# Kernel tuning notes

Measured on AMD Instinct MI355X. Metric: run time of the kernel, lower is better.

## Reference

```python
import jax, jax.numpy as jnp
import numpy as np

B, T, E, V, L, BLK = 2, 2048, 1024, 32000, 12, 2048


def setup_inputs() -> dict:
    key = jax.random.key(0)
    ks = jax.random.split(key, 10)
    std = 0.005  # FHE-friendly tiny init, matches nn.init.normal_(std=0.005)
    init = lambda k, shape: jax.random.normal(k, shape, jnp.float32) * std
    return {
        "idx": jax.random.randint(ks[0], (B, T), 0, V, dtype=jnp.int32),
        "wte": init(ks[1], (V, E)),
        "wpe": init(ks[2], (BLK, E)),
        "ln1_w": jnp.ones((L, E), jnp.float32),   # FHELayerNorm weights init to ones
        "Wq": init(ks[3], (L, E, E)),
        "Wk": init(ks[4], (L, E, E)),
        "Wv": init(ks[5], (L, E, E)),
        "Wo": init(ks[6], (L, E, E)),
        "ln2_w": jnp.ones((L, E), jnp.float32),
        "fc1": init(ks[7], (L, 2 * E, E)),
        "fc2": init(ks[8], (L, E, 2 * E)),
        "lnf_w": jnp.ones((E,), jnp.float32),
        "lm_head": init(ks[9], (V, E)),
    }


def reference(idx, wte, wpe, ln1_w, Wq, Wk, Wv, Wo, ln2_w, fc1, fc2, lnf_w, lm_head):
    t = idx.shape[1]
    # embeddings, each scaled by 0.01
    x = wte[idx] * 0.01 + (wpe[:t] * 0.01)[None, :, :]  # [B,T,E]

    n_layer = ln1_w.shape[0]
    # inter-block rescale: 0.1 after every block except the last
    scales = jnp.where(jnp.arange(n_layer) < n_layer - 1, 0.1, 1.0).astype(x.dtype)

    def block(x, p):
        ln1, wq, wk, wv, wo, ln2, f1, f2, s = p
        # FHELayerNorm: pure scaling
        h = x * ln1 * 0.1
        # attention (single head over full E, softmax-free quadratic weights)
        q = jnp.einsum('bte,fe->btf', h, wq) * 0.01
        k = jnp.einsum('bte,fe->btf', h, wk) * 0.01
        v = jnp.einsum('bte,fe->btf', h, wv) * 0.1
        a = jnp.einsum('btf,bsf->bts', q, k) * 0.01      # [B,T,T]
        a = a * a * 0.1 + a * 0.1                         # pointwise quadratic
        ao = jnp.einsum('bts,bsf->btf', a, v) * 0.01
        attn_out = jnp.einsum('btf,ef->bte', ao, wo) * 0.1
        x = (x * 0.5 + attn_out * 0.5) * 0.1
        # MLP with polynomial activation
        h2 = x * ln2 * 0.1
        m = jnp.einsum('bte,fe->btf', h2, f1) * 0.05      # [B,T,2E]
        m = m * m * 0.1 + m * 0.1
        m = jnp.einsum('btf,ef->bte', m, f2) * 0.05
        x = (x * 0.5 + m * 0.5) * 0.1
        return x * s, None

    x, _ = jax.lax.scan(block, x, (ln1_w, Wq, Wk, Wv, Wo, ln2_w, fc1, fc2, scales))
    x = x * lnf_w * 0.1  # final FHELayerNorm
    logits = jnp.einsum('bte,ve->btv', x, lm_head) * 0.5
    return logits
```

## Files before the change

kernel.cpp:

```cpp
#include <hip/hip_runtime.h>
#include <hip/hip_fp8.h>
#include <stdint.h>
#include <math.h>

typedef unsigned short u16;
typedef __attribute__((ext_vector_type(4))) float f32x4;
typedef __attribute__((ext_vector_type(2))) long long llx2;

typedef __attribute__((address_space(1))) const uint32_t gas_u32;
typedef __attribute__((address_space(3))) uint32_t las_u32;

__device__ __forceinline__ uint8_t f8(float x) {
  __hip_fp8_e4m3 t(x);
  return (uint8_t)t.__x;
}
__device__ __forceinline__ int ipos(int k) {
  return (k & ~63) | (k & 7) | ((k & 32) >> 2) | ((k & 24) << 1);
}

__device__ __forceinline__ void gl_lds16(const void* g, void* l) {
  __builtin_amdgcn_global_load_lds((gas_u32*)g, (las_u32*)l, 16, 0, 0);
}
__device__ __forceinline__ void barrier_raw() {
  asm volatile("" ::: "memory");
  __builtin_amdgcn_s_barrier();
  asm volatile("" ::: "memory");
}

#define MM8(A_, B_, C_) __builtin_amdgcn_mfma_f32_16x16x32_fp8_fp8(A_, B_, C_, 0, 0, 0)

#define PHASE_MID() do { \
  asm volatile("s_waitcnt lgkmcnt(0)" ::: "memory"); \
  __builtin_amdgcn_sched_barrier(0); \
  __builtin_amdgcn_s_setprio(1); \
} while (0)
#define PHASE_END() do { \
  __builtin_amdgcn_s_setprio(0); \
  __builtin_amdgcn_sched_barrier(0); \
  barrier_raw(); \
} while (0)

__device__ __forceinline__ void xcd_swz(int nwg, int orig, int gx, int& bx, int& by) {
  const int xcd = orig & 7, rem = orig >> 3;
  const int qq = nwg >> 3, rr = nwg & 7;
  const int wg = (xcd < rr ? xcd * (qq + 1) : rr * (qq + 1) + (xcd - rr) * qq) + rem;
  bx = wg % gx; by = wg / gx;
}

struct GP8 {
  const uint8_t* A; long long asb;
  const uint8_t* B[3]; long long bsb;
  uint8_t* O[3]; long long osb;
  int K, lda, ldb, ldo;
  float m1[3], m2[3];
  int epi[3];
  int nsel, msel, nfirst;
  float qc;
  float* xres; const float* lnw; float rscale; float oscale;
  uint8_t* h8out;
  float* fout; int ldf;
};

#define S8A(q, kh, t) do { \
  gl_lds16(gA0 + (size_t)(t) * 128 + (kh) * 64, lAw + (q) * 32768 + (kh) * 8192); \
  gl_lds16(gA1 + (size_t)(t) * 128 + (kh) * 64, lAw + (q) * 32768 + (kh) * 8192 + 4096); \
} while (0)
#define S8B(q, kh, t) do { \
  gl_lds16(gB0 + (size_t)(t) * 128 + (kh) * 64, lBw + (q) * 32768 + (kh) * 8192); \
  gl_lds16(gB1 + (size_t)(t) * 128 + (kh) * 64, lBw + (q) * 32768 + (kh) * 8192 + 4096); \
} while (0)

#define MF8() do { \
  acc[0][0]=MM8(a0[0],b0[0],acc[0][0]); acc[0][0]=MM8(a0[1],b0[1],acc[0][0]); \
  acc[0][1]=MM8(a0[0],b1[0],acc[0][1]); acc[0][1]=MM8(a0[1],b1[1],acc[0][1]); \
  acc[0][2]=MM8(a0[0],b2[0],acc[0][2]); acc[0][2]=MM8(a0[1],b2[1],acc[0][2]); \
  acc[0][3]=MM8(a0[0],b3[0],acc[0][3]); acc[0][3]=MM8(a0[1],b3[1],acc[0][3]); \
  acc[1][0]=MM8(a1[0],b0[0],acc[1][0]); acc[1][0]=MM8(a1[1],b0[1],acc[1][0]); \
  acc[1][1]=MM8(a1[0],b1[0],acc[1][1]); acc[1][1]=MM8(a1[1],b1[1],acc[1][1]); \
  acc[1][2]=MM8(a1[0],b2[0],acc[1][2]); acc[1][2]=MM8(a1[1],b2[1],acc[1][2]); \
  acc[1][3]=MM8(a1[0],b3[0],acc[1][3]); acc[1][3]=MM8(a1[1],b3[1],acc[1][3]); \
  acc[2][0]=MM8(a2[0],b0[0],acc[2][0]); acc[2][0]=MM8(a2[1],b0[1],acc[2][0]); \
  acc[2][1]=MM8(a2[0],b1[0],acc[2][1]); acc[2][1]=MM8(a2[1],b1[1],acc[2][1]); \
  acc[2][2]=MM8(a2[0],b2[0],acc[2][2]); acc[2][2]=MM8(a2[1],b2[1],acc[2][2]); \
  acc[2][3]=MM8(a2[0],b3[0],acc[2][3]); acc[2][3]=MM8(a2[1],b3[1],acc[2][3]); \
  acc[3][0]=MM8(a3[0],b0[0],acc[3][0]); acc[3][0]=MM8(a3[1],b0[1],acc[3][0]); \
  acc[3][1]=MM8(a3[0],b1[0],acc[3][1]); acc[3][1]=MM8(a3[1],b1[1],acc[3][1]); \
  acc[3][2]=MM8(a3[0],b2[0],acc[3][2]); acc[3][2]=MM8(a3[1],b2[1],acc[3][2]); \
  acc[3][3]=MM8(a3[0],b3[0],acc[3][3]); acc[3][3]=MM8(a3[1],b3[1],acc[3][3]); \
} while (0)

__global__ __launch_bounds__(256, 2) void gemm8_k(GP8 p) {
  extern __shared__ __attribute__((aligned(16))) char lds[];
  const int z = blockIdx.z;
  int bx, by;
  xcd_swz(gridDim.x * gridDim.y, blockIdx.y * gridDim.x + blockIdx.x, gridDim.x, bx, by);
  const int m0 = p.nfirst ? by * 128 : bx * 128;
  const int n0 = p.nfirst ? bx * 128 : by * 128;
  const int zi = p.nsel ? (n0 >> 10) : 0;
  const int nB = p.nsel ? (n0 & 1023) : n0;
  const uint8_t* __restrict__ Ap = p.A + (size_t)z * p.asb;
  const uint8_t* __restrict__ Bp = p.B[zi] + (size_t)(p.msel ? (m0 >> 11) : z) * p.bsb;

  const int tid = threadIdx.x, wid = tid >> 6, lane = tid & 63;
  const int wm = wid >> 1, wn = wid & 1;
  const int l15 = lane & 15, l4 = lane >> 4;
  const int cswz16 = (l4 ^ ((l15 >> 1) & 3)) * 16;

  const f32x4 vzero = {0.f, 0.f, 0.f, 0.f};
  f32x4 acc[4][4];
#pragma unroll
  for (int i = 0; i < 4; ++i)
#pragma unroll
    for (int j = 0; j < 4; ++j) acc[i][j] = vzero;

  const int sr = lane >> 2;
  const int cgB = ((lane & 3) ^ ((lane >> 3) & 3)) * 16;
  const uint8_t* gA0 = Ap + (size_t)(m0 + wid * 16 + sr) * p.lda + cgB;
  const uint8_t* gA1 = gA0 + (size_t)64 * p.lda;
  const uint8_t* gB0 = Bp + (size_t)(nB + wid * 16 + sr) * p.ldb + cgB;
  const uint8_t* gB1 = gB0 + (size_t)64 * p.ldb;
  char* lAw = lds + wid * 1024;
  char* lBw = lds + 16384 + wid * 1024;

  const int nt = p.K >> 7;

  S8A(0, 0, 0); S8B(0, 0, 0); S8A(0, 1, 0); S8B(0, 1, 0);
  S8A(1, 0, 1); S8B(1, 0, 1);
  asm volatile("s_waitcnt vmcnt(4)" ::: "memory");
  barrier_raw();

  llx2 a0, a1, a2, a3, b0, b1, b2, b3;
  for (int t = 0; t < nt; ++t) {
    const int q = t & 1;
    const char* Abase = lds + q * 32768 + (wm * 64 + l15) * 64 + cswz16;
    const char* Bbase = lds + q * 32768 + 16384 + (wn * 64 + l15) * 64 + cswz16;
    a0 = *(const llx2*)Abase;          a1 = *(const llx2*)(Abase + 1024);
    a2 = *(const llx2*)(Abase + 2048); a3 = *(const llx2*)(Abase + 3072);
    b0 = *(const llx2*)Bbase;          b1 = *(const llx2*)(Bbase + 1024);
    b2 = *(const llx2*)(Bbase + 2048); b3 = *(const llx2*)(Bbase + 3072);
    if (t + 1 < nt) { S8A(q ^ 1, 1, t + 1); S8B(q ^ 1, 1, t + 1); }
    PHASE_MID(); MF8(); PHASE_END();
    a0 = *(const llx2*)(Abase + 8192);        a1 = *(const llx2*)(Abase + 8192 + 1024);
    a2 = *(const llx2*)(Abase + 8192 + 2048); a3 = *(const llx2*)(Abase + 8192 + 3072);
    b0 = *(const llx2*)(Bbase + 8192);        b1 = *(const llx2*)(Bbase + 8192 + 1024);
    b2 = *(const llx2*)(Bbase + 8192 + 2048); b3 = *(const llx2*)(Bbase + 8192 + 3072);
    if (t + 2 < nt) { S8A(q, 0, t + 2); S8B(q, 0, t + 2); }
    PHASE_MID(); MF8();
    __builtin_amdgcn_s_setprio(0);
    __builtin_amdgcn_sched_barrier(0);
    if (t + 2 < nt) asm volatile("s_waitcnt vmcnt(4)" ::: "memory");
    else            asm volatile("s_waitcnt vmcnt(0)" ::: "memory");
    barrier_raw();
  }

  const int epi = p.epi[zi];
  const float m1v = p.m1[zi], m2v = p.m2[zi];
  uint8_t* __restrict__ Op = p.O[zi] + (size_t)z * p.osb;
#pragma unroll
  for (int mi = 0; mi < 4; ++mi) {
    const int rbase = m0 + wm * 64 + mi * 16 + l4 * 4;
#pragma unroll
    for (int ni = 0; ni < 4; ++ni) {
      const int col = nB + wn * 64 + ni * 16 + l15;
      f32x4 v = acc[mi][ni];
      if (epi == 0) {
#pragma unroll
        for (int r = 0; r < 4; ++r) {
          float y = (v[r] * m1v) * m2v;
          Op[(size_t)(rbase + r) * p.ldo + ipos(col)] = f8(y);
        }
      } else if (epi == 1) {
        const int b = rbase >> 11, rb = rbase & 2047;
        uint32_t pk = 0;
#pragma unroll
        for (int r = 0; r < 4; ++r) {
          float y = (v[r] * m1v) * m2v;
          pk |= (uint32_t)f8(y) << (8 * r);
        }
        *(uint32_t*)(Op + (size_t)b * 2097152 + (size_t)col * 2048 + ipos(rb)) = pk;
      } else if (epi == 2) {
#pragma unroll
        for (int r = 0; r < 4; ++r) {
          float u = (v[r] * m1v) * m2v;
          Op[(size_t)(rbase + r) * p.ldo + ipos(col)] = f8(u * u * p.qc + u);
        }
      } else if (epi == 3) {
#pragma unroll
        for (int r = 0; r < 4; ++r) {
          float add = (v[r] * m1v) * m2v;
          size_t ix = (size_t)(rbase + r) * 1024 + col;
          float xn = (p.xres[ix] + add) * p.rscale;
          p.xres[ix] = xn;
          float hv = xn * p.lnw[col] * 0.1f;
          p.h8out[(size_t)(rbase + r) * 1024 + ipos(col)] = f8(hv * p.oscale);
        }
      } else {
#pragma unroll
        for (int r = 0; r < 4; ++r)
          __builtin_nontemporal_store((v[r] * m1v) * m2v,
                                      &p.fout[(size_t)(rbase + r) * p.ldf + col]);
      }
    }
  }
}

#define H8STAGE(b, t) do { \
  gl_lds16(gA0 + (size_t)(t) * 128,      lds + (b) * 24576 + wid * 1024); \
  gl_lds16(gB0 + (size_t)(t) * 128,      lds + (b) * 24576 + 8192 + wid * 1024); \
  gl_lds16(gB1 + (size_t)(t) * 128,      lds + (b) * 24576 + 12288 + wid * 1024); \
  gl_lds16(gA0 + (size_t)(t) * 128 + 64, lds + (b) * 24576 + 4096 + wid * 1024); \
  gl_lds16(gB0 + (size_t)(t) * 128 + 64, lds + (b) * 24576 + 16384 + wid * 1024); \
  gl_lds16(gB1 + (size_t)(t) * 128 + 64, lds + (b) * 24576 + 20480 + wid * 1024); \
} while (0)

#define MF8H(AK, BK_) do { \
  acc[0][0]=MM8(a0##AK[0],b0##BK_[0],acc[0][0]); acc[0][0]=MM8(a0##AK[1],b0##BK_[1],acc[0][0]); \
  acc[0][1]=MM8(a0##AK[0],b1##BK_[0],acc[0][1]); acc[0][1]=MM8(a0##AK[1],b1##BK_[1],acc[0][1]); \
  acc[0][2]=MM8(a0##AK[0],b2##BK_[0],acc[0][2]); acc[0][2]=MM8(a0##AK[1],b2##BK_[1],acc[0][2]); \
  acc[0][3]=MM8(a0##AK[0],b3##BK_[0],acc[0][3]); acc[0][3]=MM8(a0##AK[1],b3##BK_[1],acc[0][3]); \
  acc[1][0]=MM8(a1##AK[0],b0##BK_[0],acc[1][0]); acc[1][0]=MM8(a1##AK[1],b0##BK_[1],acc[1][0]); \
  acc[1][1]=MM8(a1##AK[0],b1##BK_[0],acc[1][1]); acc[1][1]=MM8(a1##AK[1],b1##BK_[1],acc[1][1]); \
  acc[1][2]=MM8(a1##AK[0],b2##BK_[0],acc[1][2]); acc[1][2]=MM8(a1##AK[1],b2##BK_[1],acc[1][2]); \
  acc[1][3]=MM8(a1##AK[0],b3##BK_[0],acc[1][3]); acc[1][3]=MM8(a1##AK[1],b3##BK_[1],acc[1][3]); \
} while (0)

__global__ __launch_bounds__(256, 2) void gemm8h_k(GP8 p) {
  extern __shared__ __attribute__((aligned(16))) char lds[];
  const int z = blockIdx.z;
  int bx, by;
  xcd_swz(gridDim.x * gridDim.y, blockIdx.y * gridDim.x + blockIdx.x, gridDim.x, bx, by);
  const int m0 = bx * 64, n0 = by * 128;
  const int zi = p.nsel ? (n0 >> 10) : 0;
  const int nB = p.nsel ? (n0 & 1023) : n0;
  const uint8_t* __restrict__ Ap = p.A + (size_t)z * p.asb;
  const uint8_t* __restrict__ Bp = p.B[zi] + (size_t)(p.msel ? (m0 >> 11) : z) * p.bsb;

  const int tid = threadIdx.x, wid = tid >> 6, lane = tid & 63;
  const int wm = wid >> 1, wn = wid & 1;
  const int l15 = lane & 15, l4 = lane >> 4;
  const int cswz16 = (l4 ^ ((l15 >> 1) & 3)) * 16;

  const f32x4 vzero = {0.f, 0.f, 0.f, 0.f};
  f32x4 acc[2][4];
#pragma unroll
  for (int i = 0; i < 2; ++i)
#pragma unroll
    for (int j = 0; j < 4; ++j) acc[i][j] = vzero;

  const int sr = lane >> 2;
  const int cgB = ((lane & 3) ^ ((lane >> 3) & 3)) * 16;
  const uint8_t* gA0 = Ap + (size_t)(m0 + wid * 16 + sr) * p.lda + cgB;
  const uint8_t* gB0 = Bp + (size_t)(nB + wid * 16 + sr) * p.ldb + cgB;
  const uint8_t* gB1 = gB0 + (size_t)64 * p.ldb;

  const int nt = p.K >> 7;

  H8STAGE(0, 0);
  H8STAGE(1, 1);
  asm volatile("s_waitcnt vmcnt(6)" ::: "memory");
  barrier_raw();

  int q = 0;
  for (int t = 0; t < nt; ++t) {
    const int bn = (q == 0) ? 2 : q - 1;
    const char* Abase = lds + q * 24576 + (wm * 32 + l15) * 64 + cswz16;
    const char* Bbase = lds + q * 24576 + 8192 + (wn * 64 + l15) * 64 + cswz16;
    llx2 a0k0 = *(const llx2*)Abase;
    llx2 a1k0 = *(const llx2*)(Abase + 1024);
    llx2 a0k1 = *(const llx2*)(Abase + 4096);
    llx2 a1k1 = *(const llx2*)(Abase + 4096 + 1024);
    llx2 b0k0 = *(const llx2*)Bbase;
    llx2 b1k0 = *(const llx2*)(Bbase + 1024);
    llx2 b2k0 = *(const llx2*)(Bbase + 2048);
    llx2 b3k0 = *(const llx2*)(Bbase + 3072);
    llx2 b0k1 = *(const llx2*)(Bbase + 8192);
    llx2 b1k1 = *(const llx2*)(Bbase + 8192 + 1024);
    llx2 b2k1 = *(const llx2*)(Bbase + 8192 + 2048);
    llx2 b3k1 = *(const llx2*)(Bbase + 8192 + 3072);
    if (t + 2 < nt) H8STAGE(bn, t + 2);
    asm volatile("s_waitcnt lgkmcnt(0)" ::: "memory");
    __builtin_amdgcn_sched_barrier(0);
    __builtin_amdgcn_s_setprio(1);
    MF8H(k0, k0);
    MF8H(k1, k1);
    __builtin_amdgcn_s_setprio(0);
    __builtin_amdgcn_sched_barrier(0);
    if (t + 2 < nt) asm volatile("s_waitcnt vmcnt(6)" ::: "memory");
    else            asm volatile("s_waitcnt vmcnt(0)" ::: "memory");
    barrier_raw();
    q = (q == 2) ? 0 : q + 1;
  }

  const int epi = p.epi[zi];
  const float m1v = p.m1[zi], m2v = p.m2[zi];
  uint8_t* __restrict__ Op = p.O[zi] + (size_t)z * p.osb;
#pragma unroll
  for (int mi = 0; mi < 2; ++mi) {
    const int rbase = m0 + wm * 32 + mi * 16 + l4 * 4;
#pragma unroll
    for (int ni = 0; ni < 4; ++ni) {
      const int col = nB + wn * 64 + ni * 16 + l15;
      f32x4 v = acc[mi][ni];
      if (epi == 0) {
#pragma unroll
        for (int r = 0; r < 4; ++r) {
          float y = (v[r] * m1v) * m2v;
          Op[(size_t)(rbase + r) * p.ldo + ipos(col)] = f8(y);
        }
      } else if (epi == 1) {
        const int b = rbase >> 11, rb = rbase & 2047;
        uint32_t pk = 0;
#pragma unroll
        for (int r = 0; r < 4; ++r) {
          float y = (v[r] * m1v) * m2v;
          pk |= (uint32_t)f8(y) << (8 * r);
        }
        *(uint32_t*)(Op + (size_t)b * 2097152 + (size_t)col * 2048 + ipos(rb)) = pk;
      } else if (epi == 2) {
#pragma unroll
        for (int r = 0; r < 4; ++r) {
          float u = (v[r] * m1v) * m2v;
          Op[(size_t)(rbase + r) * p.ldo + ipos(col)] = f8(u * u * p.qc + u);
        }
      } else if (epi == 3) {
#pragma unroll
        for (int r = 0; r < 4; ++r) {
          float add = (v[r] * m1v) * m2v;
          size_t ix = (size_t)(rbase + r) * 1024 + col;
          float xn = (p.xres[ix] + add) * p.rscale;
          p.xres[ix] = xn;
          float hv = xn * p.lnw[col] * 0.1f;
          p.h8out[(size_t)(rbase + r) * 1024 + ipos(col)] = f8(hv * p.oscale);
        }
      } else {
#pragma unroll
        for (int r = 0; r < 4; ++r)
          __builtin_nontemporal_store((v[r] * m1v) * m2v,
                                      &p.fout[(size_t)(rbase + r) * p.ldf + col]);
      }
    }
  }
}

__global__ __launch_bounds__(256) void embed8_k(const int* __restrict__ idx, const float* __restrict__ wte,
                                                const float* __restrict__ wpe, const float* __restrict__ ln1,
                                                float* __restrict__ x, uint8_t* __restrict__ h8, float sh) {
  const int bt = blockIdx.x;
  const int t = bt & 2047;
  const int tok = idx[bt];
  const int e = threadIdx.x * 4;
  const float4 wv = *(const float4*)(wte + (size_t)tok * 1024 + e);
  const float4 pv = *(const float4*)(wpe + (size_t)t * 1024 + e);
  const float4 lv = *(const float4*)(ln1 + e);
  float4 xo;
  xo.x = (wv.x + pv.x) * 0.01f;
  xo.y = (wv.y + pv.y) * 0.01f;
  xo.z = (wv.z + pv.z) * 0.01f;
  xo.w = (wv.w + pv.w) * 0.01f;
  *(float4*)(x + (size_t)bt * 1024 + e) = xo;
  uint32_t pk = (uint32_t)f8(xo.x * lv.x * 0.1f * sh)
              | ((uint32_t)f8(xo.y * lv.y * 0.1f * sh) << 8)
              | ((uint32_t)f8(xo.z * lv.z * 0.1f * sh) << 16)
              | ((uint32_t)f8(xo.w * lv.w * 0.1f * sh) << 24);
  *(uint32_t*)(h8 + (size_t)bt * 1024 + ipos(e)) = pk;
}

__global__ __launch_bounds__(256) void cvtT8_k(const float* __restrict__ src, uint8_t* __restrict__ dst,
                                               float scale) {
  __shared__ float tl[64][68];
  const int z = blockIdx.z;
  const int c0 = blockIdx.x * 64, r0 = blockIdx.y * 64;
  const int tid = threadIdx.x;
  const float* s = src + (size_t)z * 1048576;
#pragma unroll
  for (int it = 0; it < 4; ++it) {
    const int r = it * 16 + (tid >> 4);
    const int c4 = (tid & 15) * 4;
    const float4 v = *(const float4*)(s + (size_t)(r0 + r) * 1024 + c0 + c4);
    tl[r][c4] = v.x; tl[r][c4 + 1] = v.y; tl[r][c4 + 2] = v.z; tl[r][c4 + 3] = v.w;
  }
  __syncthreads();
  const int c = tid >> 2;
  const int rr = (tid & 3) * 16;
  const int base = r0 + rr;
  const int O = (base & ~63) | ((base & 32) >> 2) | ((base & 16) << 1);
  uint8_t* d = dst + (size_t)z * 1048576 + (size_t)(c0 + c) * 1024 + O;
  uint32_t w0 = 0, w1 = 0, w2 = 0, w3 = 0;
#pragma unroll
  for (int j = 0; j < 4; ++j) w0 |= (uint32_t)f8(tl[rr + j][c] * scale) << (8 * j);
#pragma unroll
  for (int j = 0; j < 4; ++j) w1 |= (uint32_t)f8(tl[rr + 4 + j][c] * scale) << (8 * j);
#pragma unroll
  for (int j = 0; j < 4; ++j) w2 |= (uint32_t)f8(tl[rr + 8 + j][c] * scale) << (8 * j);
#pragma unroll
  for (int j = 0; j < 4; ++j) w3 |= (uint32_t)f8(tl[rr + 12 + j][c] * scale) << (8 * j);
  *(uint32_t*)d = w0;        *(uint32_t*)(d + 4) = w1;
  *(uint32_t*)(d + 16) = w2; *(uint32_t*)(d + 20) = w3;
}

__global__ __launch_bounds__(256) void cvtf8i_k(const float* __restrict__ src, uint8_t* __restrict__ dst,
                                                long long n, float scale) {
  long long i = ((long long)blockIdx.x * 256 + threadIdx.x) * 8;
  const long long stride = (long long)gridDim.x * 256 * 8;
  for (; i < n; i += stride) {
    const float4 a = *(const float4*)(src + i);
    const float4 b = *(const float4*)(src + i + 4);
    uint32_t lo = (uint32_t)f8(a.x * scale) | ((uint32_t)f8(a.y * scale) << 8)
                | ((uint32_t)f8(a.z * scale) << 16) | ((uint32_t)f8(a.w * scale) << 24);
    uint32_t hi = (uint32_t)f8(b.x * scale) | ((uint32_t)f8(b.y * scale) << 8)
                | ((uint32_t)f8(b.z * scale) << 16) | ((uint32_t)f8(b.w * scale) << 24);
    uint8_t* d = dst + ((i & ~63ll) | (((i >> 3) & 3) << 4) | (((i >> 5) & 1) << 3));
    *(uint32_t*)d = lo;
    *(uint32_t*)(d + 4) = hi;
  }
}

__global__ __launch_bounds__(256) void megacvt8_k(const float* __restrict__ wq, const float* __restrict__ wk,
                                                  const float* __restrict__ f1, const float* __restrict__ f2,
                                                  uint8_t* __restrict__ dst, float scale) {
  const long long M1 = 1ll << 20;
  const long long per = 6 * M1;
  const long long total = 12 * per;
  long long i = ((long long)blockIdx.x * 256 + threadIdx.x) * 8;
  const long long stride = (long long)gridDim.x * 256 * 8;
  for (; i < total; i += stride) {
    const long long l = i / per;
    const long long off = i - l * per;
    const float* s; long long so;
    if      (off < M1)     { s = wq; so = l * M1 + off; }
    else if (off < 2 * M1) { s = wk; so = l * M1 + off - M1; }
    else if (off < 4 * M1) { s = f1; so = l * 2 * M1 + off - 2 * M1; }
    else                   { s = f2; so = l * 2 * M1 + off - 4 * M1; }
    const float4 a = *(const float4*)(s + so);
    const float4 b = *(const float4*)(s + so + 4);
    uint32_t lo = (uint32_t)f8(a.x * scale) | ((uint32_t)f8(a.y * scale) << 8)
                | ((uint32_t)f8(a.z * scale) << 16) | ((uint32_t)f8(a.w * scale) << 24);
    uint32_t hi = (uint32_t)f8(b.x * scale) | ((uint32_t)f8(b.y * scale) << 8)
                | ((uint32_t)f8(b.z * scale) << 16) | ((uint32_t)f8(b.w * scale) << 24);
    uint8_t* d = dst + ((i & ~63ll) | (((i >> 3) & 3) << 4) | (((i >> 5) & 1) << 3));
    *(uint32_t*)d = lo;
    *(uint32_t*)(d + 4) = hi;
  }
}

static inline double scp(double sigma) {
  double e = round(log2(0.5 / sigma));
  if (e > 120.0) e = 120.0;
  if (e < -120.0) e = -120.0;
  return ldexp(1.0, (int)e);
}
static inline void split2(double v, float& a, float& b) {
  if (v == 0.0) { a = 0.f; b = 0.f; return; }
  int e; frexp(v, &e);
  int h = e / 2;
  a = (float)ldexp(1.0, h);
  b = (float)ldexp(v, -h);
}

extern "C" void kernel_launch(void* const* d_in, const int* in_sizes, int n_in,
                              void* d_out, int out_size, void* d_ws, size_t ws_size,
                              hipStream_t stream) {
  const int*   idx  = (const int*)  d_in[0];
  const float* wte  = (const float*)d_in[1];
  const float* wpe  = (const float*)d_in[2];
  const float* ln1w = (const float*)d_in[3];
  const float* Wq   = (const float*)d_in[4];
  const float* Wk   = (const float*)d_in[5];
  const float* Wv   = (const float*)d_in[6];
  const float* Wo   = (const float*)d_in[7];
  const float* ln2w = (const float*)d_in[8];
  const float* fc1  = (const float*)d_in[9];
  const float* fc2  = (const float*)d_in[10];
  const float* lnfw = (const float*)d_in[11];
  const float* lmh  = (const float*)d_in[12];
  float* out = (float*)d_out;

  double dSh1[12], dSqk[12], dSaq[12], dSu[12], dSh2[12], dSmq[12], dShF;
  {
    double sx = 7e-5;
    for (int l = 0; l < 12; ++l) {
      double sh1 = sx * 0.1;
      double sq  = sh1 * 0.005 * 32.0 * 0.01;
      double saq = 32.0 * sq * sq * 0.01 * 0.1;
      double su  = sh1 * 8e-4 * 32.0 * 0.1;
      double sx2 = sx * 0.05;
      double sh2 = sx2 * 0.1;
      double smq = sh2 * 0.005 * 32.0 * 0.05 * 0.1;
      dSh1[l] = scp(sh1); dSqk[l] = scp(sq); dSaq[l] = scp(saq);
      dSu[l] = scp(su); dSh2[l] = scp(sh2); dSmq[l] = scp(smq);
      sx = sx2 * 0.05 * (l < 11 ? 0.1 : 1.0);
    }
    dShF = scp(sx * 0.1);
  }
  const double SW = 128.0, SWVO = 512.0, SF = 128.0, SL = 128.0;

  char* w = (char*)d_ws;
  float*   x    = (float*)w;    w += (size_t)4096 * 1024 * 4;
  uint8_t* h8   = (uint8_t*)w;  w += (size_t)4096 * 1024;
  uint8_t* q8   = (uint8_t*)w;  w += (size_t)4096 * 1024;
  uint8_t* k8   = (uint8_t*)w;  w += (size_t)4096 * 1024;
  uint8_t* uT8  = (uint8_t*)w;  w += (size_t)2 * 1024 * 2048;
  uint8_t* a8   = (uint8_t*)w;  w += (size_t)2 * 2048 * 2048;
  uint8_t* mb8  = (uint8_t*)w;  w += (size_t)4096 * 2048;
  uint8_t* lw8  = (uint8_t*)w;  w += (size_t)12 * 6291456;
  uint8_t* wvo8 = (uint8_t*)w;  w += (size_t)12 * 1048576;
  uint8_t* lmh8 = q8;
  uint8_t* wvT8 = lw8;
  uint8_t* wo8  = lw8 + 25165824;

  const size_t SH8 = 65536, SHH = 73728;

  embed8_k<<<4096, 256, 0, stream>>>(idx, wte, wpe, ln1w, x, h8, (float)dSh1[0]);

  cvtT8_k<<<dim3(16, 16, 12), 256, 0, stream>>>(Wv, wvT8, (float)SW);
  cvtf8i_k<<<2048, 256, 0, stream>>>(Wo, wo8, 12ll * 1048576, (float)SW);
  {
    GP8 p{};
    p.A = wo8; p.asb = 1048576;
    p.B[0] = wvT8; p.bsb = 1048576;
    p.O[0] = wvo8; p.osb = 1048576;
    p.K = 1024; p.lda = 1024; p.ldb = 1024; p.ldo = 1024;
    split2(SWVO / (SW * SW), p.m1[0], p.m2[0]);
    p.epi[0] = 0;
    gemm8_k<<<dim3(8, 8, 12), 256, SH8, stream>>>(p);
  }
  megacvt8_k<<<2048, 256, 0, stream>>>(Wq, Wk, fc1, fc2, lw8, (float)SW);

  for (int l = 0; l < 12; ++l) {
    uint8_t* lwl = lw8 + (size_t)l * 6291456;
    {
      GP8 p{};
      p.A = h8; p.asb = 0;
      p.B[0] = lwl; p.B[1] = lwl + 1048576; p.B[2] = wvo8 + (size_t)l * 1048576; p.bsb = 0;
      p.O[0] = q8; p.O[1] = k8; p.O[2] = uT8; p.osb = 0;
      p.K = 1024; p.lda = 1024; p.ldb = 1024; p.ldo = 1024;
      split2(0.01 * dSqk[l] / (dSh1[l] * SW), p.m1[0], p.m2[0]);
      p.m1[1] = p.m1[0]; p.m2[1] = p.m2[0];
      split2(0.1 * dSu[l] / (dSh1[l] * SWVO), p.m1[2], p.m2[2]);
      p.epi[0] = 0; p.epi[1] = 0; p.epi[2] = 1;
      p.nsel = 1;
      gemm8_k<<<dim3(32, 24, 1), 256, SH8, stream>>>(p);
    }
    {
      GP8 p{};
      p.A = q8; p.asb = 2097152;
      p.B[0] = k8; p.bsb = 2097152;
      p.O[0] = a8; p.osb = 4194304;
      p.K = 1024; p.lda = 1024; p.ldb = 1024; p.ldo = 2048;
      split2(0.001 * dSaq[l] / (dSqk[l] * dSqk[l]), p.m1[0], p.m2[0]);
      p.qc = (float)(10.0 / dSaq[l]);
      p.epi[0] = 2;
      gemm8_k<<<dim3(16, 16, 2), 256, SH8, stream>>>(p);
    }
    {
      GP8 p{};
      p.A = a8; p.asb = 0;
      p.B[0] = uT8; p.bsb = 2097152; p.msel = 1;
      p.O[0] = a8; p.osb = 0;
      p.K = 2048; p.lda = 2048; p.ldb = 2048; p.ldo = 1024;
      split2(0.001 / (dSaq[l] * dSu[l]), p.m1[0], p.m2[0]);
      p.epi[0] = 3;
      p.xres = x; p.lnw = ln2w + (size_t)l * 1024; p.rscale = 0.05f;
      p.oscale = (float)dSh2[l]; p.h8out = h8;
      gemm8h_k<<<dim3(64, 8, 1), 256, SHH, stream>>>(p);
    }
    {
      GP8 p{};
      p.A = h8; p.asb = 0;
      p.B[0] = lwl + 2097152; p.bsb = 0;
      p.O[0] = mb8; p.osb = 0;
      p.K = 1024; p.lda = 1024; p.ldb = 1024; p.ldo = 2048;
      split2(0.005 * dSmq[l] / (dSh2[l] * SF), p.m1[0], p.m2[0]);
      p.qc = (float)(10.0 / dSmq[l]);
      p.epi[0] = 2;
      gemm8_k<<<dim3(32, 16, 1), 256, SH8, stream>>>(p);
    }
    {
      GP8 p{};
      p.A = mb8; p.asb = 0;
      p.B[0] = lwl + 4194304; p.bsb = 0;
      p.O[0] = mb8; p.osb = 0;
      p.K = 2048; p.lda = 2048; p.ldb = 2048; p.ldo = 1024;
      split2(0.05 / (dSmq[l] * SF), p.m1[0], p.m2[0]);
      p.epi[0] = 3;
      p.xres = x;
      p.rscale = (l < 11) ? 0.005f : 0.05f;
      if (l < 11) { p.lnw = ln1w + (size_t)(l + 1) * 1024; p.oscale = (float)dSh1[l + 1]; }
      else        { p.lnw = lnfw; p.oscale = (float)dShF; }
      p.h8out = h8;
      gemm8h_k<<<dim3(64, 8, 1), 256, SHH, stream>>>(p);
    }
  }

  cvtf8i_k<<<2048, 256, 0, stream>>>(lmh, lmh8, 32768000ll, (float)SL);
  {
    GP8 p{};
    p.A = h8; p.asb = 0;
    p.B[0] = lmh8; p.bsb = 0;
    p.O[0] = lmh8; p.osb = 0;
    p.K = 1024; p.lda = 1024; p.ldb = 1024; p.ldo = 0;
    split2(0.5 / (dShF * SL), p.m1[0], p.m2[0]);
    p.epi[0] = 4;
    p.nfirst = 1;
    p.fout = out; p.ldf = 32000;
    gemm8_k<<<dim3(250, 32, 1), 256, SH8, stream>>>(p);
  }
}
```

Measured before the change: 1.971 ms.

## Add 256x128 FP8 GEMM for LM head and store residual in bf16

Adds a new FP8 GEMM kernel with a 256x128 tile, 32 accumulators per wave and a 3-stage global-to-LDS pipeline, and uses it for the large LM-head projection in place of the 128x128 gemm8_k. The bigger M tile raises operand reuse per LDS load for the 4096x32000 output. Separately, the fp32 residual stream x becomes bf16, halving residual read/write traffic in the embedding and residual epilogues at some accuracy risk. Epilogue code is also factored into a shared macro.

```diff
diff --git a/kernel.cpp b/kernel.cpp
--- a/kernel.cpp
+++ b/kernel.cpp
@@ -4,12 +4,21 @@
 #include <math.h>
 
 typedef unsigned short u16;
+typedef __attribute__((ext_vector_type(4))) short s16x4;
 typedef __attribute__((ext_vector_type(4))) float f32x4;
 typedef __attribute__((ext_vector_type(2))) long long llx2;
 
 typedef __attribute__((address_space(1))) const uint32_t gas_u32;
 typedef __attribute__((address_space(3))) uint32_t las_u32;
 
+__device__ __forceinline__ u16 f2b(float f) {
+  union { float f; uint32_t u; } v; v.f = f;
+  uint32_t r = v.u + 0x7FFFu + ((v.u >> 16) & 1u);
+  return (u16)(r >> 16);
+}
+__device__ __forceinline__ float b2f(u16 b) {
+  union { uint32_t u; float f; } v; v.u = ((uint32_t)b) << 16; return v.f;
+}
 __device__ __forceinline__ uint8_t f8(float x) {
   __hip_fp8_e4m3 t(x);
   return (uint8_t)t.__x;
@@ -56,10 +65,50 @@
   int epi[3];
   int nsel, msel, nfirst;
   float qc;
-  float* xres; const float* lnw; float rscale; float oscale;
+  u16* xres; const float* lnw; float rscale; float oscale;
   uint8_t* h8out;
   float* fout; int ldf;
 };
+
+#define EPI_FRAG() do { \
+  if (epi == 0) { \
+    _Pragma("unroll") \
+    for (int r = 0; r < 4; ++r) { \
+      float y = (v[r] * m1v) * m2v; \
+      Op[(size_t)(rbase + r) * p.ldo + ipos(col)] = f8(y); \
+    } \
+  } else if (epi == 1) { \
+    const int b = rbase >> 11, rb = rbase & 2047; \
+    uint32_t pk = 0; \
+    _Pragma("unroll") \
+    for (int r = 0; r < 4; ++r) { \
+      float y = (v[r] * m1v) * m2v; \
+      pk |= (uint32_t)f8(y) << (8 * r); \
+    } \
+    *(uint32_t*)(Op + (size_t)b * 2097152 + (size_t)col * 2048 + ipos(rb)) = pk; \
+  } else if (epi == 2) { \
+    _Pragma("unroll") \
+    for (int r = 0; r < 4; ++r) { \
+      float u = (v[r] * m1v) * m2v; \
+      Op[(size_t)(rbase + r) * p.ldo + ipos(col)] = f8(u * u * p.qc + u); \
+    } \
+  } else if (epi == 3) { \
+    _Pragma("unroll") \
+    for (int r = 0; r < 4; ++r) { \
+      float add = (v[r] * m1v) * m2v; \
+      size_t ix = (size_t)(rbase + r) * 1024 + col; \
+      float xn = (b2f(p.xres[ix]) + add) * p.rscale; \
+      p.xres[ix] = f2b(xn); \
+      float hv = xn * p.lnw[col] * 0.1f; \
+      p.h8out[(size_t)(rbase + r) * 1024 + ipos(col)] = f8(hv * p.oscale); \
+    } \
+  } else { \
+    _Pragma("unroll") \
+    for (int r = 0; r < 4; ++r) \
+      __builtin_nontemporal_store((v[r] * m1v) * m2v, \
+                                  &p.fout[(size_t)(rbase + r) * p.ldf + col]); \
+  } \
+} while (0)
 
 #define S8A(q, kh, t) do { \
   gl_lds16(gA0 + (size_t)(t) * 128 + (kh) * 64, lAw + (q) * 32768 + (kh) * 8192); \
@@ -163,43 +212,7 @@
     for (int ni = 0; ni < 4; ++ni) {
       const int col = nB + wn * 64 + ni * 16 + l15;
       f32x4 v = acc[mi][ni];
-      if (epi == 0) {
-#pragma unroll
-        for (int r = 0; r < 4; ++r) {
-          float y = (v[r] * m1v) * m2v;
-          Op[(size_t)(rbase + r) * p.ldo + ipos(col)] = f8(y);
-        }
-      } else if (epi == 1) {
-        const int b = rbase >> 11, rb = rbase & 2047;
-        uint32_t pk = 0;
-#pragma unroll
-        for (int r = 0; r < 4; ++r) {
-          float y = (v[r] * m1v) * m2v;
-          pk |= (uint32_t)f8(y) << (8 * r);
-        }
-        *(uint32_t*)(Op + (size_t)b * 2097152 + (size_t)col * 2048 + ipos(rb)) = pk;
-      } else if (epi == 2) {
-#pragma unroll
-        for (int r = 0; r < 4; ++r) {
-          float u = (v[r] * m1v) * m2v;
-          Op[(size_t)(rbase + r) * p.ldo + ipos(col)] = f8(u * u * p.qc + u);
-        }
-      } else if (epi == 3) {
-#pragma unroll
-        for (int r = 0; r < 4; ++r) {
-          float add = (v[r] * m1v) * m2v;
-          size_t ix = (size_t)(rbase + r) * 1024 + col;
-          float xn = (p.xres[ix] + add) * p.rscale;
-          p.xres[ix] = xn;
-          float hv = xn * p.lnw[col] * 0.1f;
-          p.h8out[(size_t)(rbase + r) * 1024 + ipos(col)] = f8(hv * p.oscale);
-        }
-      } else {
-#pragma unroll
-        for (int r = 0; r < 4; ++r)
-          __builtin_nontemporal_store((v[r] * m1v) * m2v,
-                                      &p.fout[(size_t)(rbase + r) * p.ldf + col]);
-      }
+      EPI_FRAG();
     }
   }
 }
@@ -301,50 +314,105 @@
     for (int ni = 0; ni < 4; ++ni) {
       const int col = nB + wn * 64 + ni * 16 + l15;
       f32x4 v = acc[mi][ni];
-      if (epi == 0) {
-#pragma unroll
-        for (int r = 0; r < 4; ++r) {
-          float y = (v[r] * m1v) * m2v;
-          Op[(size_t)(rbase + r) * p.ldo + ipos(col)] = f8(y);
-        }
-      } else if (epi == 1) {
-        const int b = rbase >> 11, rb = rbase & 2047;
-        uint32_t pk = 0;
-#pragma unroll
-        for (int r = 0; r < 4; ++r) {
-          float y = (v[r] * m1v) * m2v;
-          pk |= (uint32_t)f8(y) << (8 * r);
-        }
-        *(uint32_t*)(Op + (size_t)b * 2097152 + (size_t)col * 2048 + ipos(rb)) = pk;
-      } else if (epi == 2) {
-#pragma unroll
-        for (int r = 0; r < 4; ++r) {
-          float u = (v[r] * m1v) * m2v;
-          Op[(size_t)(rbase + r) * p.ldo + ipos(col)] = f8(u * u * p.qc + u);
-        }
-      } else if (epi == 3) {
-#pragma unroll
-        for (int r = 0; r < 4; ++r) {
-          float add = (v[r] * m1v) * m2v;
-          size_t ix = (size_t)(rbase + r) * 1024 + col;
-          float xn = (p.xres[ix] + add) * p.rscale;
-          p.xres[ix] = xn;
-          float hv = xn * p.lnw[col] * 0.1f;
-          p.h8out[(size_t)(rbase + r) * 1024 + ipos(col)] = f8(hv * p.oscale);
-        }
-      } else {
-#pragma unroll
-        for (int r = 0; r < 4; ++r)
-          __builtin_nontemporal_store((v[r] * m1v) * m2v,
-                                      &p.fout[(size_t)(rbase + r) * p.ldf + col]);
+      EPI_FRAG();
+    }
+  }
+}
+
+#define P8SA(b, t) do { \
+  gl_lds16(gA0 + (size_t)(t) * 64,              lds + (b) * 24576 + wid * 1024); \
+  gl_lds16(gA0 + (size_t)(t) * 64 + arow64,     lds + (b) * 24576 + 4096 + wid * 1024); \
+  gl_lds16(gA0 + (size_t)(t) * 64 + 2 * arow64, lds + (b) * 24576 + 8192 + wid * 1024); \
+  gl_lds16(gA0 + (size_t)(t) * 64 + 3 * arow64, lds + (b) * 24576 + 12288 + wid * 1024); \
+} while (0)
+#define P8SB(b, t) do { \
+  gl_lds16(gB0 + (size_t)(t) * 64,          lds + (b) * 24576 + 16384 + wid * 1024); \
+  gl_lds16(gB0 + (size_t)(t) * 64 + brow64, lds + (b) * 24576 + 20480 + wid * 1024); \
+} while (0)
+
+__global__ __launch_bounds__(256, 2) void gemm8p_k(GP8 p) {
+  extern __shared__ __attribute__((aligned(16))) char lds[];
+  const int z = blockIdx.z;
+  int bx, by;
+  xcd_swz(gridDim.x * gridDim.y, blockIdx.y * gridDim.x + blockIdx.x, gridDim.x, bx, by);
+  const int n0 = bx * 128, m0 = by * 256;
+  const int zi = 0;
+  const uint8_t* __restrict__ Ap = p.A;
+  const uint8_t* __restrict__ Bp = p.B[0];
+
+  const int tid = threadIdx.x, wid = tid >> 6, lane = tid & 63;
+  const int wm = wid >> 1, wn = wid & 1;
+  const int l15 = lane & 15, l4 = lane >> 4;
+  const int cswz16 = (l4 ^ ((l15 >> 1) & 3)) * 16;
+
+  const f32x4 vzero = {0.f, 0.f, 0.f, 0.f};
+  f32x4 acc[8][4];
+#pragma unroll
+  for (int i = 0; i < 8; ++i)
+#pragma unroll
+    for (int j = 0; j < 4; ++j) acc[i][j] = vzero;
+
+  const int sr = lane >> 2;
+  const int cgB = ((lane & 3) ^ ((lane >> 3) & 3)) * 16;
+  const uint8_t* gA0 = Ap + (size_t)(m0 + wid * 16 + sr) * p.lda + cgB;
+  const uint8_t* gB0 = Bp + (size_t)(n0 + wid * 16 + sr) * p.ldb + cgB;
+  const size_t arow64 = (size_t)64 * p.lda;
+  const size_t brow64 = (size_t)64 * p.ldb;
+
+  const int nt = p.K >> 6;
+
+  P8SA(0, 0); P8SB(0, 0);
+  P8SA(1, 1); P8SB(1, 1);
+  asm volatile("s_waitcnt vmcnt(6)" ::: "memory");
+  barrier_raw();
+
+  int q = 0;
+  for (int t = 0; t < nt; ++t) {
+    const int bn = (q == 0) ? 2 : q - 1;
+    const char* Abase = lds + q * 24576 + (wm * 128 + l15) * 64 + cswz16;
+    const char* Bbase = lds + q * 24576 + 16384 + (wn * 64 + l15) * 64 + cswz16;
+    llx2 av[8], bv[4];
+#pragma unroll
+    for (int mi = 0; mi < 8; ++mi) av[mi] = *(const llx2*)(Abase + mi * 1024);
+#pragma unroll
+    for (int ni = 0; ni < 4; ++ni) bv[ni] = *(const llx2*)(Bbase + ni * 1024);
+    if (t + 2 < nt) { P8SA(bn, t + 2); P8SB(bn, t + 2); }
+    asm volatile("s_waitcnt lgkmcnt(0)" ::: "memory");
+    __builtin_amdgcn_sched_barrier(0);
+    __builtin_amdgcn_s_setprio(1);
+#pragma unroll
+    for (int mi = 0; mi < 8; ++mi)
+#pragma unroll
+      for (int ni = 0; ni < 4; ++ni) {
+        acc[mi][ni] = MM8(av[mi][0], bv[ni][0], acc[mi][ni]);
+        acc[mi][ni] = MM8(av[mi][1], bv[ni][1], acc[mi][ni]);
       }
+    __builtin_amdgcn_s_setprio(0);
+    __builtin_amdgcn_sched_barrier(0);
+    if (t + 2 < nt) asm volatile("s_waitcnt vmcnt(6)" ::: "memory");
+    else            asm volatile("s_waitcnt vmcnt(0)" ::: "memory");
+    barrier_raw();
+    q = (q == 2) ? 0 : q + 1;
+  }
+
+  const int epi = p.epi[zi];
+  const float m1v = p.m1[zi], m2v = p.m2[zi];
+  uint8_t* __restrict__ Op = p.O[zi];
+#pragma unroll
+  for (int mi = 0; mi < 8; ++mi) {
+    const int rbase = m0 + wm * 128 + mi * 16 + l4 * 4;
+#pragma unroll
+    for (int ni = 0; ni < 4; ++ni) {
+      const int col = n0 + wn * 64 + ni * 16 + l15;
+      f32x4 v = acc[mi][ni];
+      EPI_FRAG();
     }
   }
 }
 
 __global__ __launch_bounds__(256) void embed8_k(const int* __restrict__ idx, const float* __restrict__ wte,
                                                 const float* __restrict__ wpe, const float* __restrict__ ln1,
-                                                float* __restrict__ x, uint8_t* __restrict__ h8, float sh) {
+                                                u16* __restrict__ x, uint8_t* __restrict__ h8, float sh) {
   const int bt = blockIdx.x;
   const int t = bt & 2047;
   const int tok = idx[bt];
@@ -357,7 +425,10 @@
   xo.y = (wv.y + pv.y) * 0.01f;
   xo.z = (wv.z + pv.z) * 0.01f;
   xo.w = (wv.w + pv.w) * 0.01f;
-  *(float4*)(x + (size_t)bt * 1024 + e) = xo;
+  s16x4 xb;
+  xb[0] = (short)f2b(xo.x); xb[1] = (short)f2b(xo.y);
+  xb[2] = (short)f2b(xo.z); xb[3] = (short)f2b(xo.w);
+  *(s16x4*)(x + (size_t)bt * 1024 + e) = xb;
   uint32_t pk = (uint32_t)f8(xo.x * lv.x * 0.1f * sh)
               | ((uint32_t)f8(xo.y * lv.y * 0.1f * sh) << 8)
               | ((uint32_t)f8(xo.z * lv.z * 0.1f * sh) << 16)
@@ -495,7 +566,7 @@
   const double SW = 128.0, SWVO = 512.0, SF = 128.0, SL = 128.0;
 
   char* w = (char*)d_ws;
-  float*   x    = (float*)w;    w += (size_t)4096 * 1024 * 4;
+  u16*     x    = (u16*)w;      w += (size_t)4096 * 1024 * 2;
   uint8_t* h8   = (uint8_t*)w;  w += (size_t)4096 * 1024;
   uint8_t* q8   = (uint8_t*)w;  w += (size_t)4096 * 1024;
   uint8_t* k8   = (uint8_t*)w;  w += (size_t)4096 * 1024;
@@ -601,8 +672,7 @@
     p.K = 1024; p.lda = 1024; p.ldb = 1024; p.ldo = 0;
     split2(0.5 / (dShF * SL), p.m1[0], p.m2[0]);
     p.epi[0] = 4;
-    p.nfirst = 1;
     p.fout = out; p.ldf = 32000;
-    gemm8_k<<<dim3(250, 32, 1), 256, SH8, stream>>>(p);
-  }
-}
+    gemm8p_k<<<dim3(250, 16, 1), 256, SHH, stream>>>(p);
+  }
+}
```

Result: faster. 1.871 ms (-5.1%).
